# Performance work log

Hardware: AMD Instinct MI355X
Metric: run time of the kernel (lower is better)

## Reference

```python
import jax, jax.numpy as jnp
import numpy as np

DIM = 384
HEADS = 6
NEG = -1e9  # masked-score fill; equivalent to gathering only kept K/V rows


def setup_inputs() -> dict:
    key = jax.random.key(0)
    ks = jax.random.split(key, 9)
    B, N, C = 1, 4098, DIM
    x = jax.random.normal(ks[0], (B, N, C), dtype=jnp.float32)
    pos = jax.random.normal(ks[1], (B, N + 1, C), dtype=jnp.float32)
    # float mask in [0,1); >=0.5 means 'foreground / keep as key', <0.5 pooled into back token
    mask = jax.random.uniform(ks[2], (B, 1, N - 2), dtype=jnp.float32)
    mask_block = jnp.ones((N + 1,), dtype=jnp.float32)  # positions 0, N-1, N always kept
    Wq = jax.random.normal(ks[3], (C, C), dtype=jnp.float32) * 0.02
    Wk = jax.random.normal(ks[4], (C, C), dtype=jnp.float32) * 0.02
    Wv = jax.random.normal(ks[5], (C, C), dtype=jnp.float32) * 0.02
    Wp = jax.random.normal(ks[6], (C, C), dtype=jnp.float32) * 0.02
    bp = jnp.zeros((C,), dtype=jnp.float32)
    return {"x": x, "pos": pos, "mask": mask, "mask_block": mask_block,
            "Wq": Wq, "Wk": Wk, "Wv": Wv, "Wp": Wp, "bp": bp}


def reference(x, pos, mask, mask_block, Wq, Wk, Wv, Wp, bp):
    B, N, C = x.shape
    H = HEADS
    D = C // H
    scale = D ** -0.5
    eps = 1e-10

    # back token: average of background (mask < 0.5) interior tokens
    reverse = jnp.where(mask < 0.5, 1.0, 0.0)                      # (B,1,N-2)
    pooled = jnp.einsum('bon,bnc->boc', reverse, x[:, 1:N - 1])    # (B,1,C)
    back_tokens = pooled / (reverse.sum(axis=2, keepdims=True) + eps)

    kv_x = jnp.concatenate([x, back_tokens], axis=1)               # (B,N+1,C)
    q_x = x + pos[:, :N]
    k_x = kv_x + pos

    q = (q_x @ Wq.T).reshape(B, N, H, D).transpose(0, 2, 1, 3)       # (B,H,N,D)
    k = (k_x @ Wk.T).reshape(B, N + 1, H, D).transpose(0, 2, 1, 3)   # (B,H,N+1,D)
    v = (kv_x @ Wv.T).reshape(B, N + 1, H, D).transpose(0, 2, 1, 3)  # (B,H,N+1,D)

    # key-selection mask: original gathers rows with mask_block >= 0.5;
    # masked softmax over all N+1 keys is mathematically identical.
    mb = mask_block.at[1:N - 1].set(mask[0, 0])
    keep = mb >= 0.5                                               # (N+1,)

    scores = jnp.einsum('bhqd,bhkd->bhqk', q, k) * scale
    scores = jnp.where(keep[None, None, None, :], scores, NEG)
    attn = jax.nn.softmax(scores, axis=-1)
    out = jnp.einsum('bhqk,bhkd->bhqd', attn, v)
    out = out.transpose(0, 2, 1, 3).reshape(B, N, C)
    return out @ Wp.T + bp
```

## Files before the change

kernel.cpp:

```cpp
#include <hip/hip_runtime.h>
#include <math.h>

#define N_TOK 4098
#define NK_TOK 4099
#define C_DIM 384
#define NKPAD 4160

typedef short  bh8 __attribute__((ext_vector_type(8)));
typedef float  f32x4 __attribute__((ext_vector_type(4)));
typedef unsigned short ushort;
typedef ushort u4 __attribute__((ext_vector_type(4)));
typedef ushort u8 __attribute__((ext_vector_type(8)));

static __device__ __forceinline__ ushort f2bf(float f) {
  unsigned int u = __float_as_uint(f);
  u = (u + 0x7FFF + ((u >> 16) & 1)) >> 16;
  return (ushort)u;
}
static __device__ __forceinline__ float bf2f(ushort s) {
  return __uint_as_float(((unsigned int)s) << 16);
}

__global__ __launch_bounds__(384) void pool_kernel(
    const float* __restrict__ x, const float* __restrict__ mask,
    float* __restrict__ pooled_part, float* __restrict__ cnt_part) {
  const int b = blockIdx.x, t = threadIdx.x;
  const int r0 = b * 32;
  float acc = 0.f;
  int lc = 0;
  for (int r = r0; r < r0 + 32; ++r)
    if (mask[r] < 0.5f) { acc += x[(size_t)(r + 1) * C_DIM + t]; ++lc; }
  pooled_part[b * C_DIM + t] = acc;
  if (t == 0) cnt_part[b] = (float)lc;
}

__global__ __launch_bounds__(256) void prep_kernel(
    const float* __restrict__ x, const float* __restrict__ pos,
    const float* __restrict__ pooled_part, const float* __restrict__ cnt_part,
    const float* __restrict__ Wq, const float* __restrict__ Wk,
    const float* __restrict__ Wv, const float* __restrict__ Wp,
    const float* __restrict__ mask, const float* __restrict__ mask_block,
    ushort* __restrict__ Aq, ushort* __restrict__ Ak, ushort* __restrict__ Av,
    ushort* __restrict__ Wb, int* __restrict__ nk, int* __restrict__ inv) {
  const int b = blockIdx.x, t = threadIdx.x;
  if (b < 260) {
    __shared__ float sback[C_DIM];
    if (b == 256) {
      float cs = 0.f;
      for (int i = (t & 63); i < 128; i += 64) cs += cnt_part[i];
#pragma unroll
      for (int d = 1; d < 64; d <<= 1) cs += __shfl_xor(cs, d);
      const float ic = 1.f / (cs + 1e-10f);
      for (int c = t; c < C_DIM; c += 256) {
        float s = 0.f;
        for (int p = 0; p < 128; ++p) s += pooled_part[p * C_DIM + c];
        sback[c] = s * ic;
      }
      __syncthreads();
    }
    const int r0 = b * 16;
#pragma unroll
    for (int i = 0; i < 6; ++i) {
      const int idx = i * 1024 + t * 4;
      const int row = r0 + idx / C_DIM, col = idx % C_DIM;
      if (row >= NK_TOK) continue;
      const float4 pv = *(const float4*)&pos[(size_t)row * C_DIM + col];
      float4 xv;
      if (row == NK_TOK - 1)
        xv = make_float4(sback[col], sback[col + 1], sback[col + 2], sback[col + 3]);
      else
        xv = *(const float4*)&x[(size_t)row * C_DIM + col];
      if (row < N_TOK) {
        u4 q4 = {f2bf((xv.x + pv.x) * 0.125f), f2bf((xv.y + pv.y) * 0.125f),
                 f2bf((xv.z + pv.z) * 0.125f), f2bf((xv.w + pv.w) * 0.125f)};
        *(u4*)&Aq[(size_t)row * C_DIM + col] = q4;
      }
      u4 k4 = {f2bf(xv.x + pv.x), f2bf(xv.y + pv.y),
               f2bf(xv.z + pv.z), f2bf(xv.w + pv.w)};
      *(u4*)&Ak[(size_t)row * C_DIM + col] = k4;
      u4 v4 = {f2bf(xv.x), f2bf(xv.y), f2bf(xv.z), f2bf(xv.w)};
      *(u4*)&Av[(size_t)row * C_DIM + col] = v4;
    }
  } else if (b < 292) {
    const int wi = b - 260;
    const float* src = (wi < 8) ? Wq : (wi < 16) ? Wk : (wi < 24) ? Wv : Wp;
    const int base = (wi >> 3) * 147456 + (wi & 7) * 18432;
#pragma unroll 2
    for (int i = 0; i < 18; ++i) {
      const int g = base + i * 1024 + t * 4;
      const float4 v = *(const float4*)&src[(wi & 7) * 18432 + i * 1024 + t * 4];
      u4 o = {f2bf(v.x), f2bf(v.y), f2bf(v.z), f2bf(v.w)};
      *(u4*)&Wb[g] = o;
    }
  } else {
    __shared__ int scnt[256];
    const int j0 = t * 17;
    unsigned int bits = 0;
    int c = 0;
#pragma unroll 1
    for (int u = 0; u < 17; ++u) {
      const int j = j0 + u;
      bool keep = false;
      if (j < NK_TOK)
        keep = (j >= 1 && j <= N_TOK - 2) ? (mask[j - 1] >= 0.5f)
                                          : (mask_block[j] >= 0.5f);
      if (keep) { bits |= 1u << u; ++c; }
    }
    scnt[t] = c;
    __syncthreads();
    for (int d = 1; d < 256; d <<= 1) {
      const int v = scnt[t];
      const int add = (t >= d) ? scnt[t - d] : 0;
      __syncthreads();
      scnt[t] = v + add;
      __syncthreads();
    }
    int base = scnt[t] - c;
    if (t == 255) *nk = scnt[255];
#pragma unroll 1
    for (int u = 0; u < 17; ++u) {
      const int j = j0 + u;
      if (j < NK_TOK) inv[j] = ((bits >> u) & 1) ? base++ : -1;
    }
  }
}

static __device__ __forceinline__ void gemm_core(
    const ushort* __restrict__ A, const ushort* __restrict__ B,
    ushort (* __restrict__ As)[72], ushort (* __restrict__ Bs)[72],
    int t, int w, int quad, int l15, f32x4 acc[4]) {
  const int g = t & 7;
  u8 ra[2], rb[2];
#pragma unroll
  for (int it = 0; it < 2; ++it) {
    const int r = it * 32 + (t >> 3);
    ra[it] = *(const u8*)&A[r * C_DIM + g * 8];
    rb[it] = *(const u8*)&B[r * C_DIM + g * 8];
  }
#pragma unroll 1
  for (int kt = 0; kt < 6; ++kt) {
    __syncthreads();
#pragma unroll
    for (int it = 0; it < 2; ++it) {
      const int r = it * 32 + (t >> 3);
      *(u8*)&As[r][g * 8] = ra[it];
      *(u8*)&Bs[r][g * 8] = rb[it];
    }
    __syncthreads();
    if (kt < 5) {
      const int k0 = (kt + 1) * 64;
#pragma unroll
      for (int it = 0; it < 2; ++it) {
        const int r = it * 32 + (t >> 3);
        ra[it] = *(const u8*)&A[r * C_DIM + k0 + g * 8];
        rb[it] = *(const u8*)&B[r * C_DIM + k0 + g * 8];
      }
    }
    const bh8 b0 = *(const bh8*)&Bs[w * 16 + l15][quad * 8];
    const bh8 b1 = *(const bh8*)&Bs[w * 16 + l15][32 + quad * 8];
#pragma unroll
    for (int mb = 0; mb < 4; ++mb) {
      const bh8 a0 = *(const bh8*)&As[mb * 16 + l15][quad * 8];
      const bh8 a1 = *(const bh8*)&As[mb * 16 + l15][32 + quad * 8];
      acc[mb] = __builtin_amdgcn_mfma_f32_16x16x32_bf16(a0, b0, acc[mb], 0, 0, 0);
      acc[mb] = __builtin_amdgcn_mfma_f32_16x16x32_bf16(a1, b1, acc[mb], 0, 0, 0);
    }
  }
}

__global__ __launch_bounds__(256) void gemm3_kernel(
    const ushort* __restrict__ Aq, const ushort* __restrict__ Ak,
    const ushort* __restrict__ Av, const ushort* __restrict__ Wb,
    const int* __restrict__ inv, ushort* __restrict__ Qh,
    ushort* __restrict__ Kc, ushort* __restrict__ Vc) {
  __shared__ ushort As[64][72], Bs[64][72];
  const int t = threadIdx.x, w = t >> 6, lane = t & 63;
  const int quad = lane >> 4, l15 = lane & 15;
  const int m0 = blockIdx.x * 64;
  const int which = blockIdx.y / 6, h = blockIdx.y % 6;
  const ushort* A = (which == 0 ? Aq : which == 1 ? Ak : Av) + (size_t)m0 * C_DIM;
  const ushort* B = Wb + (size_t)which * 147456 + (size_t)h * 64 * C_DIM;
  f32x4 acc[4];
#pragma unroll
  for (int i = 0; i < 4; ++i) acc[i] = (f32x4){0.f, 0.f, 0.f, 0.f};
  gemm_core(A, B, As, Bs, t, w, quad, l15, acc);
  const int n = w * 16 + l15;
  if (which == 0) {
#pragma unroll
    for (int mb = 0; mb < 4; ++mb)
#pragma unroll
      for (int r = 0; r < 4; ++r) {
        const int m = m0 + mb * 16 + quad * 4 + r;
        if (m < N_TOK) Qh[((size_t)h * N_TOK + m) * 64 + n] = f2bf(acc[mb][r]);
      }
  } else {
    ushort* dst = (which == 1) ? Kc : Vc;
#pragma unroll
    for (int mb = 0; mb < 4; ++mb)
#pragma unroll
      for (int r = 0; r < 4; ++r) {
        const int m = m0 + mb * 16 + quad * 4 + r;
        if (m < NK_TOK) {
          const int slot = inv[m];
          if (slot >= 0) dst[((size_t)h * NKPAD + slot) * 64 + n] = f2bf(acc[mb][r]);
        }
      }
  }
}

__global__ __launch_bounds__(256) void gemm_out_kernel(
    const ushort* __restrict__ Am, const ushort* __restrict__ Wpb,
    const float* __restrict__ bp, float* __restrict__ out) {
  __shared__ ushort As[64][72], Bs[64][72];
  const int t = threadIdx.x, w = t >> 6, lane = t & 63;
  const int quad = lane >> 4, l15 = lane & 15;
  const int m0 = blockIdx.x * 64;
  const int h = blockIdx.y;
  f32x4 acc[4];
#pragma unroll
  for (int i = 0; i < 4; ++i) acc[i] = (f32x4){0.f, 0.f, 0.f, 0.f};
  gemm_core(Am + (size_t)m0 * C_DIM, Wpb + (size_t)h * 64 * C_DIM,
            As, Bs, t, w, quad, l15, acc);
  const int n = w * 16 + l15;
  const float bb = bp[h * 64 + n];
#pragma unroll
  for (int mb = 0; mb < 4; ++mb)
#pragma unroll
    for (int r = 0; r < 4; ++r) {
      const int m = m0 + mb * 16 + quad * 4 + r;
      if (m < N_TOK) out[(size_t)m * C_DIM + h * 64 + n] = acc[mb][r] + bb;
    }
}

__global__ __launch_bounds__(256) void vtrans_kernel(const ushort* __restrict__ Vc,
                                                     ushort* __restrict__ Vt) {
  __shared__ ushort T[64][72];
  const int c = blockIdx.x, h = blockIdx.y, t = threadIdx.x;
#pragma unroll
  for (int i = 0; i < 2; ++i) {
    const int s = t + i * 256, r = s >> 3, g = s & 7;
    *(u8*)&T[r][g * 8] =
        *(const u8*)&Vc[((size_t)h * NKPAD + c * 64 + r) * 64 + g * 8];
  }
  __syncthreads();
#pragma unroll
  for (int i = 0; i < 2; ++i) {
    const int s = t + i * 256, d = s >> 3, g = s & 7;
    u8 o;
#pragma unroll
    for (int j = 0; j < 8; ++j) o[j] = T[g * 8 + j][d];
    *(u8*)&Vt[((size_t)h * 64 + d) * NKPAD + c * 64 + g * 8] = o;
  }
}

__global__ __launch_bounds__(256) void attn_kernel(
    const ushort* __restrict__ Qh, const ushort* __restrict__ Kc,
    const ushort* __restrict__ Vt, const int* __restrict__ nkp,
    ushort* __restrict__ Opart, float* __restrict__ Lpart) {
  __shared__ ushort Ks[64][72];
  __shared__ ushort Vs[64][72];
  __shared__ ushort Ps[4][16][72];
  const int t = threadIdx.x, w = t >> 6, lane = t & 63;
  const int quad = lane >> 4, l15 = lane & 15;
  const int h = blockIdx.y, slice = blockIdx.z;
  const int q0 = blockIdx.x * 64;
  const int nk = *nkp, nchunk = (nk + 63) >> 6;
  const int g = t & 7;

  bh8 qf0, qf1;
  {
    int qr = q0 + w * 16 + l15;
    if (qr > N_TOK - 1) qr = N_TOK - 1;
    const ushort* qp = Qh + ((size_t)h * N_TOK + qr) * 64 + quad * 8;
    qf0 = *(const bh8*)qp;
    qf1 = *(const bh8*)(qp + 32);
  }
  f32x4 oacc[4];
#pragma unroll
  for (int i = 0; i < 4; ++i) oacc[i] = (f32x4){0.f, 0.f, 0.f, 0.f};
  float l_r = 0.f;

  const ushort* kb = Kc + (size_t)h * NKPAD * 64;
  const ushort* vb = Vt + (size_t)h * 64 * NKPAD;

  u8 rk[2], rv[2];
  if (slice < nchunk) {
#pragma unroll
    for (int it = 0; it < 2; ++it) {
      const int r = it * 32 + (t >> 3);
      rk[it] = *(const u8*)&kb[(size_t)(slice * 64 + r) * 64 + g * 8];
      rv[it] = *(const u8*)&vb[(size_t)r * NKPAD + slice * 64 + g * 8];
    }
  }
#pragma unroll 1
  for (int kc = slice; kc < nchunk; kc += 3) {
    __syncthreads();
#pragma unroll
    for (int it = 0; it < 2; ++it) {
      const int r = it * 32 + (t >> 3);
      *(u8*)&Ks[r][g * 8] = rk[it];
      *(u8*)&Vs[r][g * 8] = rv[it];
    }
    __syncthreads();
    if (kc + 3 < nchunk) {
#pragma unroll
      for (int it = 0; it < 2; ++it) {
        const int r = it * 32 + (t >> 3);
        rk[it] = *(const u8*)&kb[(size_t)((kc + 3) * 64 + r) * 64 + g * 8];
        rv[it] = *(const u8*)&vb[(size_t)r * NKPAD + (kc + 3) * 64 + g * 8];
      }
    }
    float csum = 0.f;
#pragma unroll
    for (int f = 0; f < 4; ++f) {
      f32x4 s4 = {0.f, 0.f, 0.f, 0.f};
      const bh8 a0 = *(const bh8*)&Ks[f * 16 + l15][quad * 8];
      const bh8 a1 = *(const bh8*)&Ks[f * 16 + l15][32 + quad * 8];
      s4 = __builtin_amdgcn_mfma_f32_16x16x32_bf16(a0, qf0, s4, 0, 0, 0);
      s4 = __builtin_amdgcn_mfma_f32_16x16x32_bf16(a1, qf1, s4, 0, 0, 0);
      const int keyb = kc * 64 + f * 16 + quad * 4;
      u4 pv;
#pragma unroll
      for (int r = 0; r < 4; ++r) {
        const float p = (keyb + r < nk) ? __expf(s4[r]) : 0.f;
        csum += p;
        pv[r] = f2bf(p);
      }
      *(u4*)&Ps[w][l15][f * 16 + quad * 4] = pv;
    }
    csum += __shfl_xor(csum, 16);
    csum += __shfl_xor(csum, 32);
    l_r += csum;

    const bh8 pa0 = *(const bh8*)&Ps[w][l15][quad * 8];
    const bh8 pa1 = *(const bh8*)&Ps[w][l15][32 + quad * 8];
#pragma unroll
    for (int db = 0; db < 4; ++db) {
      const bh8 b0 = *(const bh8*)&Vs[db * 16 + l15][quad * 8];
      const bh8 b1 = *(const bh8*)&Vs[db * 16 + l15][32 + quad * 8];
      oacc[db] = __builtin_amdgcn_mfma_f32_16x16x32_bf16(pa0, b0, oacc[db], 0, 0, 0);
      oacc[db] = __builtin_amdgcn_mfma_f32_16x16x32_bf16(pa1, b1, oacc[db], 0, 0, 0);
    }
  }

  const int sh = slice * 6 + h;
  const int qg = q0 + w * 16;
#pragma unroll
  for (int db = 0; db < 4; ++db)
#pragma unroll
    for (int r = 0; r < 4; ++r) {
      const int q = qg + quad * 4 + r;
      if (q < N_TOK)
        Opart[((size_t)sh * NKPAD + q) * 64 + db * 16 + l15] = f2bf(oacc[db][r]);
    }
  if (quad == 0) {
    const int q = qg + l15;
    if (q < N_TOK) Lpart[sh * NKPAD + q] = l_r;
  }
}

__global__ __launch_bounds__(256) void merge_kernel(const ushort* __restrict__ Opart,
                                                    const float* __restrict__ Lpart,
                                                    ushort* __restrict__ Am) {
  const int idx = blockIdx.x * 256 + threadIdx.x;
  if (idx >= N_TOK * 48) return;
  const int q = idx / 48, c = (idx % 48) * 8;
  const int h = c >> 6, d = c & 63;
  float l = 0.f;
#pragma unroll
  for (int s = 0; s < 3; ++s) l += Lpart[(s * 6 + h) * NKPAD + q];
  const float inv = 1.f / l;
  float o[8] = {0.f, 0.f, 0.f, 0.f, 0.f, 0.f, 0.f, 0.f};
#pragma unroll
  for (int s = 0; s < 3; ++s) {
    const u8 v = *(const u8*)&Opart[((size_t)(s * 6 + h) * NKPAD + q) * 64 + d];
#pragma unroll
    for (int j = 0; j < 8; ++j) o[j] += bf2f(v[j]);
  }
  u8 r;
#pragma unroll
  for (int j = 0; j < 8; ++j) r[j] = f2bf(o[j] * inv);
  *(u8*)&Am[(size_t)q * C_DIM + c] = r;
}

extern "C" void kernel_launch(void* const* d_in, const int* in_sizes, int n_in,
                              void* d_out, int out_size, void* d_ws, size_t ws_size,
                              hipStream_t stream) {
  const float* x          = (const float*)d_in[0];
  const float* pos        = (const float*)d_in[1];
  const float* mask       = (const float*)d_in[2];
  const float* mask_block = (const float*)d_in[3];
  const float* Wq         = (const float*)d_in[4];
  const float* Wk         = (const float*)d_in[5];
  const float* Wv         = (const float*)d_in[6];
  const float* Wp         = (const float*)d_in[7];
  const float* bp         = (const float*)d_in[8];
  float* out = (float*)d_out;
  char* wsb = (char*)d_ws;

  float*  pooled_part = (float*)wsb;
  float*  cnt_part    = (float*)(wsb + 196608);
  int*    nk          = (int*)(wsb + 197120);
  int*    inv         = (int*)(wsb + 197632);
  ushort* Aq          = (ushort*)(wsb + 215296);
  ushort* Ak          = (ushort*)(wsb + 3410176);
  ushort* Av          = (ushort*)(wsb + 6605056);
  ushort* Wb          = (ushort*)(wsb + 9799936);
  ushort* Qh          = (ushort*)(wsb + 10979584);
  ushort* Kc          = (ushort*)(wsb + 14126848);
  ushort* Vc          = (ushort*)(wsb + 17321728);
  ushort* Vt          = (ushort*)(wsb + 20516608);
  float*  Lp          = (float*)(wsb + 23711488);
  ushort* Am          = (ushort*)(wsb + 24011008);
  ushort* Op          = Aq;

  pool_kernel<<<dim3(128), dim3(384), 0, stream>>>(x, mask, pooled_part, cnt_part);
  prep_kernel<<<dim3(293), dim3(256), 0, stream>>>(x, pos, pooled_part, cnt_part,
                                                   Wq, Wk, Wv, Wp, mask, mask_block,
                                                   Aq, Ak, Av, Wb, nk, inv);
  gemm3_kernel<<<dim3(65, 18), 256, 0, stream>>>(Aq, Ak, Av, Wb, inv, Qh, Kc, Vc);
  vtrans_kernel<<<dim3(65, 6), 256, 0, stream>>>(Vc, Vt);
  attn_kernel<<<dim3(65, 6, 3), 256, 0, stream>>>(Qh, Kc, Vt, nk, Op, Lp);
  merge_kernel<<<dim3(769), 256, 0, stream>>>(Op, Lp, Am);
  gemm_out_kernel<<<dim3(65, 6), 256, 0, stream>>>(Am, Wb + 3 * 147456, bp, out);
}
```

Measured before the change: 160.1 us.

## Fuse pooling, V-transpose and merge stages; enlarge attention query tile

Folds the pooling pass into the prep kernel. The back-token K/V row is now computed by a dedicated extra block in the projection GEMM, so prep no longer waits on the pooled result. The Q scale moves into the GEMM epilogue, reusing the K input instead of a separate Aq buffer, and V is written directly in transposed layout, which removes vtrans_kernel. The split-K merge is fused into the output projection's A-tile load, and the attention kernel handles 128 queries per block so each K/V tile is reused twice. The aim is fewer launches and less intermediate global traffic, at the cost of strided scattered V stores and fewer attention blocks.

```diff
diff --git a/kernel.cpp b/kernel.cpp
--- a/kernel.cpp
+++ b/kernel.cpp
@@ -21,78 +21,30 @@
   return __uint_as_float(((unsigned int)s) << 16);
 }
 
-__global__ __launch_bounds__(384) void pool_kernel(
-    const float* __restrict__ x, const float* __restrict__ mask,
-    float* __restrict__ pooled_part, float* __restrict__ cnt_part) {
-  const int b = blockIdx.x, t = threadIdx.x;
-  const int r0 = b * 32;
-  float acc = 0.f;
-  int lc = 0;
-  for (int r = r0; r < r0 + 32; ++r)
-    if (mask[r] < 0.5f) { acc += x[(size_t)(r + 1) * C_DIM + t]; ++lc; }
-  pooled_part[b * C_DIM + t] = acc;
-  if (t == 0) cnt_part[b] = (float)lc;
-}
-
 __global__ __launch_bounds__(256) void prep_kernel(
     const float* __restrict__ x, const float* __restrict__ pos,
-    const float* __restrict__ pooled_part, const float* __restrict__ cnt_part,
+    const float* __restrict__ mask, const float* __restrict__ mask_block,
     const float* __restrict__ Wq, const float* __restrict__ Wk,
     const float* __restrict__ Wv, const float* __restrict__ Wp,
-    const float* __restrict__ mask, const float* __restrict__ mask_block,
-    ushort* __restrict__ Aq, ushort* __restrict__ Ak, ushort* __restrict__ Av,
-    ushort* __restrict__ Wb, int* __restrict__ nk, int* __restrict__ inv) {
+    float* __restrict__ pooled_part, float* __restrict__ cnt_part,
+    int* __restrict__ nk, int* __restrict__ inv,
+    ushort* __restrict__ Ak, ushort* __restrict__ Av, ushort* __restrict__ Wb) {
   const int b = blockIdx.x, t = threadIdx.x;
-  if (b < 260) {
-    __shared__ float sback[C_DIM];
-    if (b == 256) {
-      float cs = 0.f;
-      for (int i = (t & 63); i < 128; i += 64) cs += cnt_part[i];
-#pragma unroll
-      for (int d = 1; d < 64; d <<= 1) cs += __shfl_xor(cs, d);
-      const float ic = 1.f / (cs + 1e-10f);
-      for (int c = t; c < C_DIM; c += 256) {
-        float s = 0.f;
-        for (int p = 0; p < 128; ++p) s += pooled_part[p * C_DIM + c];
-        sback[c] = s * ic;
-      }
-      __syncthreads();
-    }
-    const int r0 = b * 16;
-#pragma unroll
-    for (int i = 0; i < 6; ++i) {
-      const int idx = i * 1024 + t * 4;
-      const int row = r0 + idx / C_DIM, col = idx % C_DIM;
-      if (row >= NK_TOK) continue;
-      const float4 pv = *(const float4*)&pos[(size_t)row * C_DIM + col];
-      float4 xv;
-      if (row == NK_TOK - 1)
-        xv = make_float4(sback[col], sback[col + 1], sback[col + 2], sback[col + 3]);
-      else
-        xv = *(const float4*)&x[(size_t)row * C_DIM + col];
-      if (row < N_TOK) {
-        u4 q4 = {f2bf((xv.x + pv.x) * 0.125f), f2bf((xv.y + pv.y) * 0.125f),
-                 f2bf((xv.z + pv.z) * 0.125f), f2bf((xv.w + pv.w) * 0.125f)};
-        *(u4*)&Aq[(size_t)row * C_DIM + col] = q4;
-      }
-      u4 k4 = {f2bf(xv.x + pv.x), f2bf(xv.y + pv.y),
-               f2bf(xv.z + pv.z), f2bf(xv.w + pv.w)};
-      *(u4*)&Ak[(size_t)row * C_DIM + col] = k4;
-      u4 v4 = {f2bf(xv.x), f2bf(xv.y), f2bf(xv.z), f2bf(xv.w)};
-      *(u4*)&Av[(size_t)row * C_DIM + col] = v4;
-    }
-  } else if (b < 292) {
-    const int wi = b - 260;
-    const float* src = (wi < 8) ? Wq : (wi < 16) ? Wk : (wi < 24) ? Wv : Wp;
-    const int base = (wi >> 3) * 147456 + (wi & 7) * 18432;
-#pragma unroll 2
-    for (int i = 0; i < 18; ++i) {
-      const int g = base + i * 1024 + t * 4;
-      const float4 v = *(const float4*)&src[(wi & 7) * 18432 + i * 1024 + t * 4];
-      u4 o = {f2bf(v.x), f2bf(v.y), f2bf(v.z), f2bf(v.w)};
-      *(u4*)&Wb[g] = o;
-    }
-  } else {
+  if (b < 128) {
+    const int r0 = b * 32;
+    float a0 = 0.f, a1 = 0.f;
+    int lc = 0;
+    for (int r = r0; r < r0 + 32; ++r) {
+      if (mask[r] < 0.5f) {
+        a0 += x[(size_t)(r + 1) * C_DIM + t];
+        if (t < 128) a1 += x[(size_t)(r + 1) * C_DIM + 256 + t];
+        ++lc;
+      }
+    }
+    pooled_part[b * C_DIM + t] = a0;
+    if (t < 128) pooled_part[b * C_DIM + 256 + t] = a1;
+    if (t == 0) cnt_part[b] = (float)lc;
+  } else if (b == 128) {
     __shared__ int scnt[256];
     const int j0 = t * 17;
     unsigned int bits = 0;
@@ -122,6 +74,31 @@
       const int j = j0 + u;
       if (j < NK_TOK) inv[j] = ((bits >> u) & 1) ? base++ : -1;
     }
+  } else if (b < 258) {
+    const int r0 = (b - 129) * 32;
+#pragma unroll 3
+    for (int i = 0; i < 12; ++i) {
+      const int idx = i * 1024 + t * 4;
+      const int row = r0 + idx / C_DIM, col = idx % C_DIM;
+      if (row >= N_TOK) continue;
+      const float4 pv = *(const float4*)&pos[(size_t)row * C_DIM + col];
+      const float4 xv = *(const float4*)&x[(size_t)row * C_DIM + col];
+      u4 k4 = {f2bf(xv.x + pv.x), f2bf(xv.y + pv.y),
+               f2bf(xv.z + pv.z), f2bf(xv.w + pv.w)};
+      *(u4*)&Ak[(size_t)row * C_DIM + col] = k4;
+      u4 v4 = {f2bf(xv.x), f2bf(xv.y), f2bf(xv.z), f2bf(xv.w)};
+      *(u4*)&Av[(size_t)row * C_DIM + col] = v4;
+    }
+  } else {
+    const int wi = b - 258;
+    const float* src = (wi < 8) ? Wq : (wi < 16) ? Wk : (wi < 24) ? Wv : Wp;
+    const int base = (wi >> 3) * 147456 + (wi & 7) * 18432;
+#pragma unroll 2
+    for (int i = 0; i < 18; ++i) {
+      const float4 v = *(const float4*)&src[(wi & 7) * 18432 + i * 1024 + t * 4];
+      u4 o = {f2bf(v.x), f2bf(v.y), f2bf(v.z), f2bf(v.w)};
+      *(u4*)&Wb[base + i * 1024 + t * 4] = o;
+    }
   }
 }
 
@@ -169,16 +146,54 @@
 }
 
 __global__ __launch_bounds__(256) void gemm3_kernel(
-    const ushort* __restrict__ Aq, const ushort* __restrict__ Ak,
-    const ushort* __restrict__ Av, const ushort* __restrict__ Wb,
-    const int* __restrict__ inv, ushort* __restrict__ Qh,
-    ushort* __restrict__ Kc, ushort* __restrict__ Vc) {
+    const ushort* __restrict__ Ak, const ushort* __restrict__ Av,
+    const ushort* __restrict__ Wb, const int* __restrict__ inv,
+    const float* __restrict__ pooled_part, const float* __restrict__ cnt_part,
+    const float* __restrict__ pos, ushort* __restrict__ Qh,
+    ushort* __restrict__ Kc, ushort* __restrict__ Vt) {
   __shared__ ushort As[64][72], Bs[64][72];
+  __shared__ float skin[C_DIM], svin[C_DIM];
   const int t = threadIdx.x, w = t >> 6, lane = t & 63;
   const int quad = lane >> 4, l15 = lane & 15;
+  const int which = blockIdx.y / 6, h = blockIdx.y % 6;
+
+  if (blockIdx.x == 65) {
+    if (blockIdx.y != 0) return;
+    float cs = 0.f;
+    for (int i = 0; i < 128; ++i) cs += cnt_part[i];
+    const float ic = 1.f / (cs + 1e-10f);
+    for (int c = t; c < C_DIM; c += 256) {
+      float s = 0.f;
+      for (int p = 0; p < 128; ++p) s += pooled_part[p * C_DIM + c];
+      const float back = s * ic;
+      skin[c] = bf2f(f2bf(back + pos[(size_t)(NK_TOK - 1) * C_DIM + c]));
+      svin[c] = bf2f(f2bf(back));
+    }
+    __syncthreads();
+    const int slot = inv[NK_TOK - 1];
+    for (int o = t; o < C_DIM; o += 256) {
+      const ushort* wk = Wb + 147456 + (size_t)o * C_DIM;
+      const ushort* wv = Wb + 294912 + (size_t)o * C_DIM;
+      float ka = 0.f, va = 0.f;
+#pragma unroll 4
+      for (int c8 = 0; c8 < 48; ++c8) {
+        const u8 k8 = *(const u8*)&wk[c8 * 8];
+        const u8 v8 = *(const u8*)&wv[c8 * 8];
+#pragma unroll
+        for (int j = 0; j < 8; ++j) {
+          ka += bf2f(k8[j]) * skin[c8 * 8 + j];
+          va += bf2f(v8[j]) * svin[c8 * 8 + j];
+        }
+      }
+      const int hh = o >> 6, d = o & 63;
+      Kc[((size_t)hh * NKPAD + slot) * 64 + d] = f2bf(ka);
+      Vt[((size_t)(hh * 64 + d)) * NKPAD + slot] = f2bf(va);
+    }
+    return;
+  }
+
   const int m0 = blockIdx.x * 64;
-  const int which = blockIdx.y / 6, h = blockIdx.y % 6;
-  const ushort* A = (which == 0 ? Aq : which == 1 ? Ak : Av) + (size_t)m0 * C_DIM;
+  const ushort* A = (which == 2 ? Av : Ak) + (size_t)m0 * C_DIM;
   const ushort* B = Wb + (size_t)which * 147456 + (size_t)h * 64 * C_DIM;
   f32x4 acc[4];
 #pragma unroll
@@ -191,65 +206,31 @@
 #pragma unroll
       for (int r = 0; r < 4; ++r) {
         const int m = m0 + mb * 16 + quad * 4 + r;
-        if (m < N_TOK) Qh[((size_t)h * N_TOK + m) * 64 + n] = f2bf(acc[mb][r]);
-      }
-  } else {
-    ushort* dst = (which == 1) ? Kc : Vc;
+        if (m < N_TOK)
+          Qh[((size_t)h * N_TOK + m) * 64 + n] = f2bf(acc[mb][r] * 0.125f);
+      }
+  } else if (which == 1) {
 #pragma unroll
     for (int mb = 0; mb < 4; ++mb)
 #pragma unroll
       for (int r = 0; r < 4; ++r) {
         const int m = m0 + mb * 16 + quad * 4 + r;
-        if (m < NK_TOK) {
+        if (m < NK_TOK - 1) {
           const int slot = inv[m];
-          if (slot >= 0) dst[((size_t)h * NKPAD + slot) * 64 + n] = f2bf(acc[mb][r]);
+          if (slot >= 0) Kc[((size_t)h * NKPAD + slot) * 64 + n] = f2bf(acc[mb][r]);
         }
       }
-  }
-}
-
-__global__ __launch_bounds__(256) void gemm_out_kernel(
-    const ushort* __restrict__ Am, const ushort* __restrict__ Wpb,
-    const float* __restrict__ bp, float* __restrict__ out) {
-  __shared__ ushort As[64][72], Bs[64][72];
-  const int t = threadIdx.x, w = t >> 6, lane = t & 63;
-  const int quad = lane >> 4, l15 = lane & 15;
-  const int m0 = blockIdx.x * 64;
-  const int h = blockIdx.y;
-  f32x4 acc[4];
-#pragma unroll
-  for (int i = 0; i < 4; ++i) acc[i] = (f32x4){0.f, 0.f, 0.f, 0.f};
-  gemm_core(Am + (size_t)m0 * C_DIM, Wpb + (size_t)h * 64 * C_DIM,
-            As, Bs, t, w, quad, l15, acc);
-  const int n = w * 16 + l15;
-  const float bb = bp[h * 64 + n];
-#pragma unroll
-  for (int mb = 0; mb < 4; ++mb)
-#pragma unroll
-    for (int r = 0; r < 4; ++r) {
-      const int m = m0 + mb * 16 + quad * 4 + r;
-      if (m < N_TOK) out[(size_t)m * C_DIM + h * 64 + n] = acc[mb][r] + bb;
-    }
-}
-
-__global__ __launch_bounds__(256) void vtrans_kernel(const ushort* __restrict__ Vc,
-                                                     ushort* __restrict__ Vt) {
-  __shared__ ushort T[64][72];
-  const int c = blockIdx.x, h = blockIdx.y, t = threadIdx.x;
-#pragma unroll
-  for (int i = 0; i < 2; ++i) {
-    const int s = t + i * 256, r = s >> 3, g = s & 7;
-    *(u8*)&T[r][g * 8] =
-        *(const u8*)&Vc[((size_t)h * NKPAD + c * 64 + r) * 64 + g * 8];
-  }
-  __syncthreads();
-#pragma unroll
-  for (int i = 0; i < 2; ++i) {
-    const int s = t + i * 256, d = s >> 3, g = s & 7;
-    u8 o;
-#pragma unroll
-    for (int j = 0; j < 8; ++j) o[j] = T[g * 8 + j][d];
-    *(u8*)&Vt[((size_t)h * 64 + d) * NKPAD + c * 64 + g * 8] = o;
+  } else {
+#pragma unroll
+    for (int mb = 0; mb < 4; ++mb)
+#pragma unroll
+      for (int r = 0; r < 4; ++r) {
+        const int m = m0 + mb * 16 + quad * 4 + r;
+        if (m < NK_TOK - 1) {
+          const int slot = inv[m];
+          if (slot >= 0) Vt[((size_t)(h * 64 + n)) * NKPAD + slot] = f2bf(acc[mb][r]);
+        }
+      }
   }
 }
 
@@ -259,26 +240,29 @@
     ushort* __restrict__ Opart, float* __restrict__ Lpart) {
   __shared__ ushort Ks[64][72];
   __shared__ ushort Vs[64][72];
-  __shared__ ushort Ps[4][16][72];
+  __shared__ ushort Ps[4][32][72];
   const int t = threadIdx.x, w = t >> 6, lane = t & 63;
   const int quad = lane >> 4, l15 = lane & 15;
   const int h = blockIdx.y, slice = blockIdx.z;
-  const int q0 = blockIdx.x * 64;
+  const int q0 = blockIdx.x * 128;
   const int nk = *nkp, nchunk = (nk + 63) >> 6;
-  const int g = t & 7;
-
-  bh8 qf0, qf1;
-  {
-    int qr = q0 + w * 16 + l15;
+  const int g8 = t & 7;
+
+  bh8 qf[2][2];
+#pragma unroll
+  for (int g = 0; g < 2; ++g) {
+    int qr = q0 + w * 32 + g * 16 + l15;
     if (qr > N_TOK - 1) qr = N_TOK - 1;
     const ushort* qp = Qh + ((size_t)h * N_TOK + qr) * 64 + quad * 8;
-    qf0 = *(const bh8*)qp;
-    qf1 = *(const bh8*)(qp + 32);
-  }
-  f32x4 oacc[4];
-#pragma unroll
-  for (int i = 0; i < 4; ++i) oacc[i] = (f32x4){0.f, 0.f, 0.f, 0.f};
-  float l_r = 0.f;
+    qf[g][0] = *(const bh8*)qp;
+    qf[g][1] = *(const bh8*)(qp + 32);
+  }
+  f32x4 oacc[2][4];
+#pragma unroll
+  for (int g = 0; g < 2; ++g)
+#pragma unroll
+    for (int i = 0; i < 4; ++i) oacc[g][i] = (f32x4){0.f, 0.f, 0.f, 0.f};
+  float l_r[2] = {0.f, 0.f};
 
   const ushort* kb = Kc + (size_t)h * NKPAD * 64;
   const ushort* vb = Vt + (size_t)h * 64 * NKPAD;
@@ -288,8 +272,8 @@
 #pragma unroll
     for (int it = 0; it < 2; ++it) {
       const int r = it * 32 + (t >> 3);
-      rk[it] = *(const u8*)&kb[(size_t)(slice * 64 + r) * 64 + g * 8];
-      rv[it] = *(const u8*)&vb[(size_t)r * NKPAD + slice * 64 + g * 8];
+      rk[it] = *(const u8*)&kb[(size_t)(slice * 64 + r) * 64 + g8 * 8];
+      rv[it] = *(const u8*)&vb[(size_t)r * NKPAD + slice * 64 + g8 * 8];
     }
   }
 #pragma unroll 1
@@ -298,89 +282,164 @@
 #pragma unroll
     for (int it = 0; it < 2; ++it) {
       const int r = it * 32 + (t >> 3);
-      *(u8*)&Ks[r][g * 8] = rk[it];
-      *(u8*)&Vs[r][g * 8] = rv[it];
+      *(u8*)&Ks[r][g8 * 8] = rk[it];
+      *(u8*)&Vs[r][g8 * 8] = rv[it];
     }
     __syncthreads();
     if (kc + 3 < nchunk) {
 #pragma unroll
       for (int it = 0; it < 2; ++it) {
         const int r = it * 32 + (t >> 3);
-        rk[it] = *(const u8*)&kb[(size_t)((kc + 3) * 64 + r) * 64 + g * 8];
-        rv[it] = *(const u8*)&vb[(size_t)r * NKPAD + (kc + 3) * 64 + g * 8];
-      }
-    }
-    float csum = 0.f;
+        rk[it] = *(const u8*)&kb[(size_t)((kc + 3) * 64 + r) * 64 + g8 * 8];
+        rv[it] = *(const u8*)&vb[(size_t)r * NKPAD + (kc + 3) * 64 + g8 * 8];
+      }
+    }
+    float csum[2] = {0.f, 0.f};
 #pragma unroll
     for (int f = 0; f < 4; ++f) {
-      f32x4 s4 = {0.f, 0.f, 0.f, 0.f};
       const bh8 a0 = *(const bh8*)&Ks[f * 16 + l15][quad * 8];
       const bh8 a1 = *(const bh8*)&Ks[f * 16 + l15][32 + quad * 8];
-      s4 = __builtin_amdgcn_mfma_f32_16x16x32_bf16(a0, qf0, s4, 0, 0, 0);
-      s4 = __builtin_amdgcn_mfma_f32_16x16x32_bf16(a1, qf1, s4, 0, 0, 0);
       const int keyb = kc * 64 + f * 16 + quad * 4;
-      u4 pv;
-#pragma unroll
-      for (int r = 0; r < 4; ++r) {
-        const float p = (keyb + r < nk) ? __expf(s4[r]) : 0.f;
-        csum += p;
-        pv[r] = f2bf(p);
-      }
-      *(u4*)&Ps[w][l15][f * 16 + quad * 4] = pv;
-    }
-    csum += __shfl_xor(csum, 16);
-    csum += __shfl_xor(csum, 32);
-    l_r += csum;
-
-    const bh8 pa0 = *(const bh8*)&Ps[w][l15][quad * 8];
-    const bh8 pa1 = *(const bh8*)&Ps[w][l15][32 + quad * 8];
+#pragma unroll
+      for (int g = 0; g < 2; ++g) {
+        f32x4 s4 = {0.f, 0.f, 0.f, 0.f};
+        s4 = __builtin_amdgcn_mfma_f32_16x16x32_bf16(a0, qf[g][0], s4, 0, 0, 0);
+        s4 = __builtin_amdgcn_mfma_f32_16x16x32_bf16(a1, qf[g][1], s4, 0, 0, 0);
+        u4 pv;
+#pragma unroll
+        for (int r = 0; r < 4; ++r) {
+          const float p = (keyb + r < nk) ? __expf(s4[r]) : 0.f;
+          csum[g] += p;
+          pv[r] = f2bf(p);
+        }
+        *(u4*)&Ps[w][g * 16 + l15][f * 16 + quad * 4] = pv;
+      }
+    }
+#pragma unroll
+    for (int g = 0; g < 2; ++g) {
+      csum[g] += __shfl_xor(csum[g], 16);
+      csum[g] += __shfl_xor(csum[g], 32);
+      l_r[g] += csum[g];
+    }
+    bh8 pa[2][2];
+#pragma unroll
+    for (int g = 0; g < 2; ++g) {
+      pa[g][0] = *(const bh8*)&Ps[w][g * 16 + l15][quad * 8];
+      pa[g][1] = *(const bh8*)&Ps[w][g * 16 + l15][32 + quad * 8];
+    }
 #pragma unroll
     for (int db = 0; db < 4; ++db) {
       const bh8 b0 = *(const bh8*)&Vs[db * 16 + l15][quad * 8];
       const bh8 b1 = *(const bh8*)&Vs[db * 16 + l15][32 + quad * 8];
-      oacc[db] = __builtin_amdgcn_mfma_f32_16x16x32_bf16(pa0, b0, oacc[db], 0, 0, 0);
-      oacc[db] = __builtin_amdgcn_mfma_f32_16x16x32_bf16(pa1, b1, oacc[db], 0, 0, 0);
+#pragma unroll
+      for (int g = 0; g < 2; ++g) {
+        oacc[g][db] = __builtin_amdgcn_mfma_f32_16x16x32_bf16(pa[g][0], b0, oacc[g][db], 0, 0, 0);
+        oacc[g][db] = __builtin_amdgcn_mfma_f32_16x16x32_bf16(pa[g][1], b1, oacc[g][db], 0, 0, 0);
+      }
     }
   }
 
   const int sh = slice * 6 + h;
-  const int qg = q0 + w * 16;
-#pragma unroll
-  for (int db = 0; db < 4; ++db)
+#pragma unroll
+  for (int g = 0; g < 2; ++g) {
+#pragma unroll
+    for (int db = 0; db < 4; ++db)
+#pragma unroll
+      for (int r = 0; r < 4; ++r) {
+        const int q = q0 + w * 32 + g * 16 + quad * 4 + r;
+        if (q < N_TOK)
+          Opart[((size_t)sh * NKPAD + q) * 64 + db * 16 + l15] = f2bf(oacc[g][db][r]);
+      }
+    if (quad == 0) {
+      const int q = q0 + w * 32 + g * 16 + l15;
+      if (q < N_TOK) Lpart[sh * NKPAD + q] = l_r[g];
+    }
+  }
+}
+
+__global__ __launch_bounds__(256) void gemm_out_kernel(
+    const ushort* __restrict__ Opart, const float* __restrict__ Lpart,
+    const ushort* __restrict__ Wpb, const float* __restrict__ bp,
+    float* __restrict__ out) {
+  __shared__ ushort As[64][72], Bs[64][72];
+  const int t = threadIdx.x, w = t >> 6, lane = t & 63;
+  const int quad = lane >> 4, l15 = lane & 15;
+  const int m0 = blockIdx.x * 64;
+  const int n0 = blockIdx.y * 64;
+  const int g8 = t & 7;
+  f32x4 acc[4];
+#pragma unroll
+  for (int i = 0; i < 4; ++i) acc[i] = (f32x4){0.f, 0.f, 0.f, 0.f};
+
+  u8 ra[2], rb[2];
+#pragma unroll
+  for (int it = 0; it < 2; ++it) {
+    const int r = it * 32 + (t >> 3), m = m0 + r;
+    float l = 0.f;
+#pragma unroll
+    for (int s = 0; s < 3; ++s) l += Lpart[(s * 6 + 0) * NKPAD + m];
+    const float invl = 1.f / l;
+    float o[8] = {0, 0, 0, 0, 0, 0, 0, 0};
+#pragma unroll
+    for (int s = 0; s < 3; ++s) {
+      const u8 v = *(const u8*)&Opart[((size_t)(s * 6 + 0) * NKPAD + m) * 64 + g8 * 8];
+#pragma unroll
+      for (int j = 0; j < 8; ++j) o[j] += bf2f(v[j]);
+    }
+#pragma unroll
+    for (int j = 0; j < 8; ++j) ra[it][j] = f2bf(o[j] * invl);
+    rb[it] = *(const u8*)&Wpb[(size_t)(n0 + r) * C_DIM + g8 * 8];
+  }
+#pragma unroll 1
+  for (int kt = 0; kt < 6; ++kt) {
+    __syncthreads();
+#pragma unroll
+    for (int it = 0; it < 2; ++it) {
+      const int r = it * 32 + (t >> 3);
+      *(u8*)&As[r][g8 * 8] = ra[it];
+      *(u8*)&Bs[r][g8 * 8] = rb[it];
+    }
+    __syncthreads();
+    if (kt < 5) {
+      const int kh = kt + 1;
+#pragma unroll
+      for (int it = 0; it < 2; ++it) {
+        const int r = it * 32 + (t >> 3), m = m0 + r;
+        float l = 0.f;
+#pragma unroll
+        for (int s = 0; s < 3; ++s) l += Lpart[(s * 6 + kh) * NKPAD + m];
+        const float invl = 1.f / l;
+        float o[8] = {0, 0, 0, 0, 0, 0, 0, 0};
+#pragma unroll
+        for (int s = 0; s < 3; ++s) {
+          const u8 v = *(const u8*)&Opart[((size_t)(s * 6 + kh) * NKPAD + m) * 64 + g8 * 8];
+#pragma unroll
+          for (int j = 0; j < 8; ++j) o[j] += bf2f(v[j]);
+        }
+#pragma unroll
+        for (int j = 0; j < 8; ++j) ra[it][j] = f2bf(o[j] * invl);
+        rb[it] = *(const u8*)&Wpb[(size_t)(n0 + r) * C_DIM + kh * 64 + g8 * 8];
+      }
+    }
+    const bh8 b0 = *(const bh8*)&Bs[w * 16 + l15][quad * 8];
+    const bh8 b1 = *(const bh8*)&Bs[w * 16 + l15][32 + quad * 8];
+#pragma unroll
+    for (int mb = 0; mb < 4; ++mb) {
+      const bh8 a0 = *(const bh8*)&As[mb * 16 + l15][quad * 8];
+      const bh8 a1 = *(const bh8*)&As[mb * 16 + l15][32 + quad * 8];
+      acc[mb] = __builtin_amdgcn_mfma_f32_16x16x32_bf16(a0, b0, acc[mb], 0, 0, 0);
+      acc[mb] = __builtin_amdgcn_mfma_f32_16x16x32_bf16(a1, b1, acc[mb], 0, 0, 0);
+    }
+  }
+  const int n = w * 16 + l15;
+  const float bb = bp[n0 + n];
+#pragma unroll
+  for (int mb = 0; mb < 4; ++mb)
 #pragma unroll
     for (int r = 0; r < 4; ++r) {
-      const int q = qg + quad * 4 + r;
-      if (q < N_TOK)
-        Opart[((size_t)sh * NKPAD + q) * 64 + db * 16 + l15] = f2bf(oacc[db][r]);
-    }
-  if (quad == 0) {
-    const int q = qg + l15;
-    if (q < N_TOK) Lpart[sh * NKPAD + q] = l_r;
-  }
-}
-
-__global__ __launch_bounds__(256) void merge_kernel(const ushort* __restrict__ Opart,
-                                                    const float* __restrict__ Lpart,
-                                                    ushort* __restrict__ Am) {
-  const int idx = blockIdx.x * 256 + threadIdx.x;
-  if (idx >= N_TOK * 48) return;
-  const int q = idx / 48, c = (idx % 48) * 8;
-  const int h = c >> 6, d = c & 63;
-  float l = 0.f;
-#pragma unroll
-  for (int s = 0; s < 3; ++s) l += Lpart[(s * 6 + h) * NKPAD + q];
-  const float inv = 1.f / l;
-  float o[8] = {0.f, 0.f, 0.f, 0.f, 0.f, 0.f, 0.f, 0.f};
-#pragma unroll
-  for (int s = 0; s < 3; ++s) {
-    const u8 v = *(const u8*)&Opart[((size_t)(s * 6 + h) * NKPAD + q) * 64 + d];
-#pragma unroll
-    for (int j = 0; j < 8; ++j) o[j] += bf2f(v[j]);
-  }
-  u8 r;
-#pragma unroll
-  for (int j = 0; j < 8; ++j) r[j] = f2bf(o[j] * inv);
-  *(u8*)&Am[(size_t)q * C_DIM + c] = r;
+      const int m = m0 + mb * 16 + quad * 4 + r;
+      if (m < N_TOK) out[(size_t)m * C_DIM + n0 + n] = acc[mb][r] + bb;
+    }
 }
 
 extern "C" void kernel_launch(void* const* d_in, const int* in_sizes, int n_in,
@@ -398,29 +457,25 @@
   float* out = (float*)d_out;
   char* wsb = (char*)d_ws;
 
-  float*  pooled_part = (float*)wsb;
-  float*  cnt_part    = (float*)(wsb + 196608);
-  int*    nk          = (int*)(wsb + 197120);
-  int*    inv         = (int*)(wsb + 197632);
-  ushort* Aq          = (ushort*)(wsb + 215296);
-  ushort* Ak          = (ushort*)(wsb + 3410176);
-  ushort* Av          = (ushort*)(wsb + 6605056);
-  ushort* Wb          = (ushort*)(wsb + 9799936);
-  ushort* Qh          = (ushort*)(wsb + 10979584);
-  ushort* Kc          = (ushort*)(wsb + 14126848);
-  ushort* Vc          = (ushort*)(wsb + 17321728);
-  ushort* Vt          = (ushort*)(wsb + 20516608);
-  float*  Lp          = (float*)(wsb + 23711488);
-  ushort* Am          = (ushort*)(wsb + 24011008);
-  ushort* Op          = Aq;
-
-  pool_kernel<<<dim3(128), dim3(384), 0, stream>>>(x, mask, pooled_part, cnt_part);
-  prep_kernel<<<dim3(293), dim3(256), 0, stream>>>(x, pos, pooled_part, cnt_part,
-                                                   Wq, Wk, Wv, Wp, mask, mask_block,
-                                                   Aq, Ak, Av, Wb, nk, inv);
-  gemm3_kernel<<<dim3(65, 18), 256, 0, stream>>>(Aq, Ak, Av, Wb, inv, Qh, Kc, Vc);
-  vtrans_kernel<<<dim3(65, 6), 256, 0, stream>>>(Vc, Vt);
-  attn_kernel<<<dim3(65, 6, 3), 256, 0, stream>>>(Qh, Kc, Vt, nk, Op, Lp);
-  merge_kernel<<<dim3(769), 256, 0, stream>>>(Op, Lp, Am);
-  gemm_out_kernel<<<dim3(65, 6), 256, 0, stream>>>(Am, Wb + 3 * 147456, bp, out);
-}
+  float*  cnt_part    = (float*)wsb;
+  int*    nk          = (int*)(wsb + 512);
+  int*    inv         = (int*)(wsb + 1024);
+  float*  pooled_part = (float*)(wsb + 20480);
+  ushort* Ak          = (ushort*)(wsb + 217088);
+  ushort* Av          = (ushort*)(wsb + 3411968);
+  ushort* Wb          = (ushort*)(wsb + 6606848);
+  ushort* Qh          = (ushort*)(wsb + 7786496);
+  ushort* Kc          = (ushort*)(wsb + 10933760);
+  ushort* Vt          = (ushort*)(wsb + 14128640);
+  ushort* Op          = (ushort*)(wsb + 17323520);
+  float*  Lp          = (float*)(wsb + 26908160);
+
+  prep_kernel<<<dim3(290), dim3(256), 0, stream>>>(
+      x, pos, mask, mask_block, Wq, Wk, Wv, Wp,
+      pooled_part, cnt_part, nk, inv, Ak, Av, Wb);
+  gemm3_kernel<<<dim3(66, 18), dim3(256), 0, stream>>>(
+      Ak, Av, Wb, inv, pooled_part, cnt_part, pos, Qh, Kc, Vt);
+  attn_kernel<<<dim3(33, 6, 3), dim3(256), 0, stream>>>(Qh, Kc, Vt, nk, Op, Lp);
+  gemm_out_kernel<<<dim3(65, 6), dim3(256), 0, stream>>>(Op, Lp, Wb + 3 * 147456,
+                                                         bp, out);
+}
```

Measured after the change: 166.8 us. 4.2% more time.
